# Optimization experiments

Hardware: AMD Instinct MI355X
Metric: run time of the kernel (lower is better)

## Reference

```python
import jax, jax.numpy as jnp
import numpy as np

N_HEADS = 16


def build_bd3lm_mask(n, block_size, dtype):
    """BD3LM mask for concatenated [xt | x0] input of length 2n.
    0 = attend, finfo.min = masked. Shape (2n, 2n)."""
    idx = jnp.arange(2 * n)
    q_idx = idx[:, None]
    kv_idx = idx[None, :]
    x0_q = q_idx >= n
    x0_kv = kv_idx >= n
    block_q = jnp.where(x0_q, (q_idx - n) // block_size, q_idx // block_size)
    block_kv = jnp.where(x0_kv, (kv_idx - n) // block_size, kv_idx // block_size)
    block_diagonal = (block_q == block_kv) & (x0_q == x0_kv)
    offset_block_causal = (block_q > block_kv) & x0_kv & (~x0_q)
    block_causal = (block_q >= block_kv) & x0_kv & x0_q
    can_attend = block_diagonal | offset_block_causal | block_causal
    neg = jnp.finfo(dtype).min
    return jnp.where(can_attend, jnp.array(0, dtype), jnp.array(neg, dtype))


def setup_inputs() -> dict:
    key = jax.random.key(0)
    ks = jax.random.split(key, 5)
    B, T, D = 4, 2048, 1024  # T = 2*L, L = 1024
    s = 1.0 / np.sqrt(D)
    return {
        "x": jax.random.normal(ks[0], (B, T, D), jnp.float32),
        "Wq": jax.random.normal(ks[1], (D, D), jnp.float32) * s,
        "bq": jnp.zeros((D,), jnp.float32),
        "Wk": jax.random.normal(ks[2], (D, D), jnp.float32) * s,
        "bk": jnp.zeros((D,), jnp.float32),
        "Wv": jax.random.normal(ks[3], (D, D), jnp.float32) * s,
        "bv": jnp.zeros((D,), jnp.float32),
        "Wo": jax.random.normal(ks[4], (D, D), jnp.float32) * s,
        "bo": jnp.zeros((D,), jnp.float32),
        "block_size": 4,
    }


def reference(x, Wq, bq, Wk, bk, Wv, bv, Wo, bo, block_size):
    B, T, D = x.shape
    H = N_HEADS
    hd = D // H
    n = T // 2  # length of each copy in [xt | x0]
    mask = build_bd3lm_mask(n, block_size, x.dtype)  # (T, T)

    def split_heads(t):  # (B, T, D) -> (B, H, T, hd)
        return t.reshape(B, T, H, hd).transpose(0, 2, 1, 3)

    q = split_heads(x @ Wq + bq) * (hd ** -0.5)
    k = split_heads(x @ Wk + bk)
    v = split_heads(x @ Wv + bv)
    scores = jnp.einsum("bhqd,bhkd->bhqk", q, k) + mask[None, None]
    attn = jax.nn.softmax(scores, axis=-1)
    ctx = jnp.einsum("bhqk,bhkd->bhqd", attn, v)
    ctx = ctx.transpose(0, 2, 1, 3).reshape(B, T, D)
    return ctx @ Wo + bo
```

## Files before the change

### kernel.cpp

```cpp
#include <hip/hip_runtime.h>
#include <hip/hip_bf16.h>
#include <stdint.h>

typedef __hip_bfloat16 bf16;
typedef short v8s __attribute__((ext_vector_type(8)));
typedef float v4f __attribute__((ext_vector_type(4)));

#define TT   2048
#define DD   1024
#define HH   16
#define HDIM 64
#define NN   1024
#define MASKV (-1e9f)
#define QSCALE 0.18033688011112042f

#if __has_builtin(__builtin_amdgcn_exp2f)
#define EXP2F(x) __builtin_amdgcn_exp2f(x)
#else
#define EXP2F(x) exp2f(x)
#endif

__device__ __forceinline__ v4f mfma16x16x32(v8s a, v8s b, v4f c) {
    return __builtin_amdgcn_mfma_f32_16x16x32_bf16(a, b, c, 0, 0, 0);
}

#define GLDS16(lds, g)                                                          \
    __builtin_amdgcn_global_load_lds(                                           \
        (const __attribute__((address_space(1))) void*)(g),                     \
        (__attribute__((address_space(3))) void*)(lds), 16, 0, 0)

__device__ __forceinline__ bf16 f2b(float f) { return __float2bfloat16(f); }

__global__ __launch_bounds__(256) void cast_x(const float* __restrict__ x,
                                              bf16* __restrict__ xb)
{
    const size_t i = ((size_t)blockIdx.x * 256 + threadIdx.x) * 4;
    const float4 f = *(const float4*)(x + i);
    union { bf16 b[4]; uint64_t u; } cv;
    cv.b[0] = f2b(f.x); cv.b[1] = f2b(f.y); cv.b[2] = f2b(f.z); cv.b[3] = f2b(f.w);
    *(uint64_t*)(xb + i) = cv.u;
}

__global__ __launch_bounds__(256) void transpose_w(
    const float* __restrict__ w0, const float* __restrict__ w1,
    const float* __restrict__ w2, const float* __restrict__ w3,
    bf16* __restrict__ dst)
{
    __shared__ float tile[64][65];
    const float* src = (blockIdx.z == 0) ? w0 : (blockIdx.z == 1) ? w1
                      : (blockIdx.z == 2) ? w2 : w3;
    bf16* d = dst + (size_t)blockIdx.z * 1024 * 1024;
    const int r0 = blockIdx.y * 64, c0 = blockIdx.x * 64;
    const int tx = threadIdx.x, ty = threadIdx.y;
#pragma unroll
    for (int j = 0; j < 16; j++) {
        int r = ty + j * 4;
        tile[r][tx] = src[(size_t)(r0 + r) * 1024 + c0 + tx];
    }
    __syncthreads();
#pragma unroll
    for (int j = 0; j < 16; j++) {
        int r = ty + j * 4;
        d[(size_t)(c0 + r) * 1024 + r0 + tx] = f2b(tile[tx][r]);
    }
}

__global__ __launch_bounds__(256) void transpose_v(
    const bf16* __restrict__ vtmp, bf16* __restrict__ vt)
{
    __shared__ bf16 tile[64][66];
    const int bh = blockIdx.y, t0 = blockIdx.x * 64;
    const int tx = threadIdx.x, ty = threadIdx.y;
    const bf16* src = vtmp + (size_t)bh * TT * HDIM;
    bf16* dst = vt + (size_t)bh * HDIM * TT;
#pragma unroll
    for (int j = 0; j < 16; j++) {
        int r = ty + j * 4;
        tile[r][tx] = src[(size_t)(t0 + r) * HDIM + tx];
    }
    __syncthreads();
#pragma unroll
    for (int j = 0; j < 16; j++) {
        int r = ty + j * 4;
        dst[(size_t)r * TT + t0 + tx] = tile[tx][r];
    }
}

__device__ __forceinline__ void gemm_core_256x128(
    const bf16* __restrict__ A, const bf16* __restrict__ BT,
    const int m0, const int n0, const int K,
    bf16* __restrict__ As, bf16* __restrict__ Bs,
    v4f (&acc)[8][2])
{
    const int tid  = threadIdx.x;
    const int lane = tid & 63, wv = tid >> 6;
    const int quad = lane >> 4, c = lane & 15;
    const int wm = wv >> 2, wn = wv & 3;
    const int c7 = c & 7;
    const int NT = K >> 6;

    const int rloc = wv * 8 + (lane >> 3);
    const int gsw  = ((lane & 7) ^ ((lane >> 3) & 7)) << 3;
    const bf16* aSrc = A  + (size_t)(m0 + rloc) * K + gsw;
    const bf16* bSrc = BT + (size_t)(n0 + rloc) * K + gsw;

#pragma unroll
    for (int i = 0; i < 8; i++)
#pragma unroll
        for (int j = 0; j < 2; j++) acc[i][j] = (v4f){0.f, 0.f, 0.f, 0.f};

    auto stageA = [&](bf16* dst, int j, int kt) {
        const int mo = ((j & 1) << 7) | ((j >> 1) << 6);
        GLDS16(dst + (j * 64 + wv * 8) * 64, aSrc + (size_t)mo * K + kt * 64);
    };
    auto stageB = [&](bf16* dst, int j, int kt) {
        GLDS16(dst + (j * 64 + wv * 8) * 64, bSrc + (size_t)(j << 6) * K + kt * 64);
    };

    stageB(Bs, 0, 0); stageB(Bs, 1, 0);
    stageA(As, 0, 0); stageA(As, 1, 0); stageA(As, 2, 0); stageA(As, 3, 0);
    asm volatile("s_waitcnt vmcnt(2)" ::: "memory");
    asm volatile("s_barrier" ::: "memory");

#pragma unroll 1
    for (int kt = 0; kt < NT; ++kt) {
        bf16* Ac = As + (kt & 1) * 16384;
        bf16* Bc = Bs + (kt & 1) * 8192;
        bf16* An = As + ((kt & 1) ^ 1) * 16384;
        bf16* Bn = Bs + ((kt & 1) ^ 1) * 8192;
        const int ktn = (kt + 1 < NT) ? kt + 1 : kt;

        v8s bfr[2][2];
#pragma unroll
        for (int nt = 0; nt < 2; nt++)
#pragma unroll
            for (int kh = 0; kh < 2; kh++)
                bfr[nt][kh] = *(const v8s*)(Bc + (wn * 32 + nt * 16 + c) * 64
                                            + (((kh * 4 + quad) ^ c7) << 3));
        v8s af[4][2];
#pragma unroll
        for (int mt = 0; mt < 4; mt++)
#pragma unroll
            for (int kh = 0; kh < 2; kh++)
                af[mt][kh] = *(const v8s*)(Ac + (wm * 64 + mt * 16 + c) * 64
                                           + (((kh * 4 + quad) ^ c7) << 3));
        stageB(Bn, 0, ktn); stageB(Bn, 1, ktn); stageA(An, 0, ktn);
        asm volatile("s_barrier" ::: "memory");
        __builtin_amdgcn_s_setprio(1);
#pragma unroll
        for (int mt = 0; mt < 4; mt++)
#pragma unroll
            for (int nt = 0; nt < 2; nt++) {
                acc[mt][nt] = mfma16x16x32(af[mt][0], bfr[nt][0], acc[mt][nt]);
                acc[mt][nt] = mfma16x16x32(af[mt][1], bfr[nt][1], acc[mt][nt]);
            }
        __builtin_amdgcn_s_setprio(0);
        asm volatile("s_waitcnt vmcnt(3)" ::: "memory");
        asm volatile("s_barrier" ::: "memory");

#pragma unroll
        for (int mt = 0; mt < 4; mt++)
#pragma unroll
            for (int kh = 0; kh < 2; kh++)
                af[mt][kh] = *(const v8s*)(Ac + (128 + wm * 64 + mt * 16 + c) * 64
                                           + (((kh * 4 + quad) ^ c7) << 3));
        stageA(An, 1, ktn); stageA(An, 2, ktn); stageA(An, 3, ktn);
        asm volatile("s_barrier" ::: "memory");
        __builtin_amdgcn_s_setprio(1);
#pragma unroll
        for (int mt = 0; mt < 4; mt++)
#pragma unroll
            for (int nt = 0; nt < 2; nt++) {
                acc[4 + mt][nt] = mfma16x16x32(af[mt][0], bfr[nt][0], acc[4 + mt][nt]);
                acc[4 + mt][nt] = mfma16x16x32(af[mt][1], bfr[nt][1], acc[4 + mt][nt]);
            }
        __builtin_amdgcn_s_setprio(0);
        asm volatile("s_waitcnt vmcnt(2)" ::: "memory");
        asm volatile("s_barrier" ::: "memory");
    }
}

__global__ __launch_bounds__(512, 2) void gemm_qkv(
    const bf16* __restrict__ A, const bf16* __restrict__ BT,
    const float* __restrict__ bq, const float* __restrict__ bk,
    const float* __restrict__ bv,
    bf16* __restrict__ qo, bf16* __restrict__ ko, bf16* __restrict__ vo)
{
    __shared__ __align__(16) bf16 As[2 * 256 * 64];
    __shared__ __align__(16) bf16 Bs[2 * 128 * 64];
    const int id  = blockIdx.x;
    const int fid = (id & 7) * 96 + (id >> 3);
    const int by  = fid / 24, bx = fid - by * 24;
    const int m0  = by * 256, n0 = bx * 128;

    v4f acc[8][2];
    gemm_core_256x128(A, BT, m0, n0, 1024, As, Bs, acc);

    const int tid  = threadIdx.x;
    const int lane = tid & 63, wv = tid >> 6;
    const int quad = lane >> 4, c = lane & 15;
    const int wm = wv >> 2, wn = wv & 3;

    const int type = n0 >> 10;
    bf16* o = (type == 0) ? qo : (type == 1) ? ko : vo;
    const float* bp = (type == 0) ? bq : (type == 1) ? bk : bv;
    const float scale = (type == 0) ? QSCALE : 1.0f;
    const int nbase = n0 & 1023;

#pragma unroll
    for (int mt = 0; mt < 8; mt++)
#pragma unroll
        for (int nt = 0; nt < 2; nt++) {
            const int within = nbase + wn * 32 + nt * 16 + c;
            const int h = within >> 6, d = within & 63;
            const float bias = bp[within];
#pragma unroll
            for (int r = 0; r < 4; r++) {
                const int row = m0 + wm * 128 + mt * 16 + quad * 4 + r;
                const int b_ = row >> 11, t = row & 2047;
                const int bh = b_ * HH + h;
                o[((size_t)bh * TT + t) * HDIM + d] =
                    f2b((acc[mt][nt][r] + bias) * scale);
            }
        }
}

__global__ __launch_bounds__(512, 2) void gemm_out(
    const bf16* __restrict__ A, const bf16* __restrict__ BT,
    const float* __restrict__ bo, float* __restrict__ out)
{
    __shared__ __align__(16) bf16 As[2 * 256 * 64];
    __shared__ __align__(16) bf16 Bs[2 * 128 * 64];
    const int id  = blockIdx.x;
    const int fid = (id & 7) * 32 + (id >> 3);
    const int by  = fid >> 3, bx = fid & 7;
    const int m0  = by * 256, n0 = bx * 128;

    v4f acc[8][2];
    gemm_core_256x128(A, BT, m0, n0, 1024, As, Bs, acc);

    const int tid  = threadIdx.x;
    const int lane = tid & 63, wv = tid >> 6;
    const int quad = lane >> 4, c = lane & 15;
    const int wm = wv >> 2, wn = wv & 3;

#pragma unroll
    for (int mt = 0; mt < 8; mt++)
#pragma unroll
        for (int nt = 0; nt < 2; nt++) {
            const int col = n0 + wn * 32 + nt * 16 + c;
            const float bias = bo[col];
#pragma unroll
            for (int r = 0; r < 4; r++) {
                const int row = m0 + wm * 128 + mt * 16 + quad * 4 + r;
                out[(size_t)row * 1024 + col] = acc[mt][nt][r] + bias;
            }
        }
}

__global__ __launch_bounds__(256, 4) void attn(
    const bf16* __restrict__ Q, const bf16* __restrict__ Kb,
    const bf16* __restrict__ VT, bf16* __restrict__ ctx,
    const int* __restrict__ bsp)
{
    __shared__ __align__(16) bf16 Kt[2][32 * 64];
    __shared__ __align__(16) bf16 Vt[2][64 * 32];
    __shared__ __align__(16) bf16 plds[4][2][16 * 32];

    const int bs = bsp[0];
    const float inv  = 1.0f / (float)bs;
    const float hinv = 0.5f * inv;
    const int tid = threadIdx.x, lane = tid & 63, wv = tid >> 6;
    const int quad = lane >> 4, c = lane & 15;
    const int bh = blockIdx.x & 63;
    const int j  = blockIdx.x >> 6;
    const int g_tbl[16] = {7,6,5,4, 0,1,2,3, 4,5,6,7, 3,2,1,0};
    const bool xt = j < 8;
    const int g  = g_tbl[j];
    const int q0g = (xt ? 0 : NN) + g * 128;

    const bf16* qp = Q  + (size_t)bh * TT * HDIM;
    const bf16* kp = Kb + (size_t)bh * TT * HDIM;
    const bf16* vp = VT + (size_t)bh * HDIM * TT;

    int d_lo = 0, nd = 0, nf = 0, b_lo = 0, nb = 0;
    if (xt) {
        d_lo = (bs * (q0g / bs)) & ~31;
        const int d_hi = min((bs * ((q0g + 127) / bs) + bs + 31) & ~31, NN);
        nd = (d_hi - d_lo) >> 5;
        const int f = bs * (q0g / bs);
        nf = f >> 5;
        b_lo = NN + (nf << 5);
        const int b_hi = NN + min((bs * ((q0g + 127) / bs) + 31) & ~31, NN);
        nb = (b_hi > b_lo) ? (b_hi - b_lo) >> 5 : 0;
    } else {
        const int q0l = q0g - NN;
        const int f = min(bs * (q0l / bs) + bs, NN);
        nf = f >> 5;
        b_lo = NN + (nf << 5);
        const int b_hi = NN + min((bs * ((q0l + 127) / bs) + bs + 31) & ~31, NN);
        nb = (b_hi > b_lo) ? (b_hi - b_lo) >> 5 : 0;
    }
    const int nc = nd + nf + nb;

    float bqv[2][4];
#pragma unroll
    for (int t = 0; t < 2; t++)
#pragma unroll
        for (int r = 0; r < 4; r++) {
            const int qrow = q0g + wv * 32 + t * 16 + quad * 4 + r;
            const int qloc = xt ? qrow : qrow - NN;
            bqv[t][r] = floorf(fmaf((float)qloc, inv, hinv));
        }

    v8s aq[2][2];
#pragma unroll
    for (int t = 0; t < 2; t++) {
        const int rowb = q0g + wv * 32 + t * 16;
        aq[t][0] = *(const v8s*)(qp + (size_t)(rowb + c) * HDIM + quad * 8);
        aq[t][1] = *(const v8s*)(qp + (size_t)(rowb + c) * HDIM + 32 + quad * 8);
    }

    v4f O[2][4];
#pragma unroll
    for (int t = 0; t < 2; t++)
#pragma unroll
        for (int dt = 0; dt < 4; dt++) O[t][dt] = (v4f){0.f, 0.f, 0.f, 0.f};
    float lr[2][4] = {{0.f,0.f,0.f,0.f},{0.f,0.f,0.f,0.f}};

    const int klrow = lane >> 3, ks8 = lane & 7;
    const bf16* kSrc0 = kp + (size_t)(wv * 8 + klrow) * HDIM + ((ks8 ^ klrow) << 3);
    const int vlrow = lane >> 2, vs8 = lane & 3;
    const bf16* vSrc0 = vp + (size_t)(wv * 16 + vlrow) * TT + ((vs8 ^ (vlrow & 3)) << 3);

    auto kb_of = [&](int i, int& kb, int& type) {
        if (i < nd)           { kb = d_lo + (i << 5);             type = 1; }
        else if (i < nd + nf) { kb = NN + ((i - nd) << 5);        type = 0; }
        else                  { kb = b_lo + ((i - nd - nf) << 5); type = xt ? 2 : 3; }
    };
    auto stage = [&](int i) {
        int kb, ty; kb_of(i, kb, ty);
        const int sel = i & 1;
        GLDS16(&Kt[sel][wv * 512], kSrc0 + (size_t)kb * HDIM);
        GLDS16(&Vt[sel][wv * 512], vSrc0 + kb);
    };

    stage(0);
    asm volatile("s_waitcnt vmcnt(0)" ::: "memory");
    asm volatile("s_barrier" ::: "memory");

    const int xk = c & 7, xv = c & 3;
    const int pquad = quad << 3;
#pragma unroll 1
    for (int i = 0; i < nc; i++) {
        int kb, type; kb_of(i, kb, type);
        const int sel = i & 1;
        const bf16* Kl = Kt[sel];
        const bf16* Vl = Vt[sel];

        const v8s k0a = *(const v8s*)(Kl + c * 64        + ((quad       ^ xk) << 3));
        const v8s k0b = *(const v8s*)(Kl + c * 64        + (((quad ^ 4) ^ xk) << 3));
        const v8s k1a = *(const v8s*)(Kl + (16 + c) * 64 + ((quad       ^ xk) << 3));
        const v8s k1b = *(const v8s*)(Kl + (16 + c) * 64 + (((quad ^ 4) ^ xk) << 3));
        v8s vf[4];
#pragma unroll
        for (int dt = 0; dt < 4; dt++)
            vf[dt] = *(const v8s*)(Vl + (dt * 16 + c) * 32 + ((quad ^ xv) << 3));

        if (i + 1 < nc) stage(i + 1);

        float bkA = 0.f, bkB = 0.f;
        if (type) {
            const int off = (type == 1) ? 0 : NN;
            bkA = floorf(fmaf((float)(kb + c - off),      inv, hinv));
            bkB = floorf(fmaf((float)(kb + 16 + c - off), inv, hinv));
        }

#pragma unroll
        for (int t = 0; t < 2; t++) {
            v4f Sa = (v4f){0.f, 0.f, 0.f, 0.f};
            v4f Sb = (v4f){0.f, 0.f, 0.f, 0.f};
            Sa = mfma16x16x32(aq[t][0], k0a, Sa);
            Sa = mfma16x16x32(aq[t][1], k0b, Sa);
            Sb = mfma16x16x32(aq[t][0], k1a, Sb);
            Sb = mfma16x16x32(aq[t][1], k1b, Sb);
            bf16* pw = &plds[wv][t][(quad * 4) * 32];
#pragma unroll
            for (int r = 0; r < 4; r++) {
                float sa = Sa[r], sb = Sb[r];
                if (type == 1) {
                    if (bkA != bqv[t][r]) sa = MASKV;
                    if (bkB != bqv[t][r]) sb = MASKV;
                } else if (type == 2) {
                    if (!(bkA < bqv[t][r])) sa = MASKV;
                    if (!(bkB < bqv[t][r])) sb = MASKV;
                } else if (type == 3) {
                    if (!(bkA <= bqv[t][r])) sa = MASKV;
                    if (!(bkB <= bqv[t][r])) sb = MASKV;
                }
                const float pa = EXP2F(sa);
                const float pb = EXP2F(sb);
                lr[t][r] += pa + pb;
                pw[r * 32 + (c ^ pquad)]        = f2b(pa);
                pw[r * 32 + ((c + 16) ^ pquad)] = f2b(pb);
            }
        }
        asm volatile("s_waitcnt lgkmcnt(0)" ::: "memory");
#pragma unroll
        for (int t = 0; t < 2; t++) {
            const v8s pf = *(const v8s*)(&plds[wv][t][c * 32 +
                                        ((quad ^ ((c >> 2) & 3)) << 3)]);
#pragma unroll
            for (int dt = 0; dt < 4; dt++)
                O[t][dt] = mfma16x16x32(pf, vf[dt], O[t][dt]);
        }

        asm volatile("s_waitcnt vmcnt(0)" ::: "memory");
        asm volatile("s_barrier" ::: "memory");
    }

    const int b_ = bh >> 4, h = bh & 15;
#pragma unroll
    for (int t = 0; t < 2; t++)
#pragma unroll
        for (int r = 0; r < 4; r++) {
            float s = lr[t][r];
#pragma unroll
            for (int off = 1; off < 16; off <<= 1) s += __shfl_xor(s, off);
            const float invl = 1.0f / fmaxf(s, 1e-30f);
            const int trow = q0g + wv * 32 + t * 16 + quad * 4 + r;
#pragma unroll
            for (int dt = 0; dt < 4; dt++)
                ctx[((size_t)(b_ * TT + trow)) * DD + h * 64 + dt * 16 + c] =
                    f2b(O[t][dt][r] * invl);
        }
}

extern "C" void kernel_launch(void* const* d_in, const int* in_sizes, int n_in,
                              void* d_out, int out_size, void* d_ws, size_t ws_size,
                              hipStream_t stream)
{
    const float* x  = (const float*)d_in[0];
    const float* Wq = (const float*)d_in[1];
    const float* bq = (const float*)d_in[2];
    const float* Wk = (const float*)d_in[3];
    const float* bk = (const float*)d_in[4];
    const float* Wv = (const float*)d_in[5];
    const float* bv = (const float*)d_in[6];
    const float* Wo = (const float*)d_in[7];
    const float* bo = (const float*)d_in[8];
    const int*  bsp = (const int*)d_in[9];
    float* out = (float*)d_out;

    bf16* ws    = (bf16*)d_ws;
    bf16* xb    = ws;
    bf16* wqkvT = xb + 8388608;
    bf16* woT   = wqkvT + 3 * 1024 * 1024;
    bf16* qbuf  = woT + 1024 * 1024;
    bf16* kbuf  = qbuf + 8388608;
    bf16* vtmp  = kbuf + 8388608;
    bf16* vt    = vtmp + 8388608;
    bf16* ctx   = xb;

    cast_x<<<8192, 256, 0, stream>>>(x, xb);
    transpose_w<<<dim3(16, 16, 4), dim3(64, 4), 0, stream>>>(Wq, Wk, Wv, Wo, wqkvT);
    gemm_qkv<<<768, 512, 0, stream>>>(xb, wqkvT, bq, bk, bv, qbuf, kbuf, vtmp);
    transpose_v<<<dim3(32, 64), dim3(64, 4), 0, stream>>>(vtmp, vt);
    attn<<<1024, 256, 0, stream>>>(qbuf, kbuf, vt, ctx, bsp);
    gemm_out<<<256, 512, 0, stream>>>(ctx, woT, bo, out);
}
```

Measured before the change: 244.6 us.

## Retile QKV GEMM to 256x192 blocks with a custom four-phase pipeline

After: 239.4 us. 2.1% less time.

```diff
diff --git a/kernel.cpp b/kernel.cpp
--- a/kernel.cpp
+++ b/kernel.cpp
@@ -86,6 +86,167 @@
     }
 }
 
+__global__ __launch_bounds__(512, 2) void gemm_qkv(
+    const bf16* __restrict__ A, const bf16* __restrict__ BT,
+    const float* __restrict__ bq, const float* __restrict__ bk,
+    const float* __restrict__ bv,
+    bf16* __restrict__ qo, bf16* __restrict__ ko, bf16* __restrict__ vo)
+{
+    __shared__ __align__(16) bf16 As[2 * 256 * 64];
+    __shared__ __align__(16) bf16 Bs[2 * 192 * 64];
+    const int K = 1024, NT = K >> 6;
+
+    const int id  = blockIdx.x;
+    const int fid = (id & 7) * 64 + (id >> 3);
+    const int by  = fid >> 4, bx = fid & 15;
+    const int m0  = by * 256, n0 = bx * 192;
+
+    const int tid  = threadIdx.x;
+    const int lane = tid & 63, wv = tid >> 6;
+    const int quad = lane >> 4, c = lane & 15;
+    const int wm = wv >> 2, wn = wv & 3;
+    const int c7 = c & 15 & 7;
+
+    const int q8  = lane >> 3;
+    const int gsw = ((lane & 7) ^ (q8 & 7)) << 3;
+    const bf16* aSrc = A + (size_t)(m0 + wv * 8 + q8) * K + gsw;
+    const int vB = wv * 8 + q8;
+    const bf16* bSrc = BT + (size_t)(n0 + (vB >> 4) * 48 + (vB & 15)) * K + gsw;
+
+    auto stageA = [&](bf16* dst, int j, int kt) {
+        GLDS16(dst + (j * 64 + wv * 8) * 64, aSrc + (size_t)(j * 64) * K + kt * 64);
+    };
+    auto stageB = [&](bf16* dst, int j, int kt) {
+        GLDS16(dst + (j * 64 + wv * 8) * 64, bSrc + (size_t)(j * 16) * K + kt * 64);
+    };
+
+    v4f acc[8][3];
+#pragma unroll
+    for (int i = 0; i < 8; i++)
+#pragma unroll
+        for (int j = 0; j < 3; j++) acc[i][j] = (v4f){0.f, 0.f, 0.f, 0.f};
+
+    stageB(Bs, 0, 0); stageB(Bs, 1, 0);
+    stageA(As, 0, 0); stageA(As, 2, 0);
+    stageA(As, 1, 0); stageA(As, 3, 0);
+    stageB(Bs, 2, 0);
+    asm volatile("s_waitcnt vmcnt(3)" ::: "memory");
+    asm volatile("s_barrier" ::: "memory");
+
+    v8s afr[4][2], bfr01[2][2], bfr2[2];
+#pragma unroll 1
+    for (int kt = 0; kt < NT; ++kt) {
+        bf16* Ac = As + (kt & 1) * 16384;
+        bf16* Bc = Bs + (kt & 1) * 12288;
+        bf16* An = As + ((kt & 1) ^ 1) * 16384;
+        bf16* Bn = Bs + ((kt & 1) ^ 1) * 12288;
+        const int ktn = (kt + 1 < NT) ? kt + 1 : kt;
+
+#pragma unroll
+        for (int nt = 0; nt < 2; nt++)
+#pragma unroll
+            for (int kh = 0; kh < 2; kh++)
+                bfr01[nt][kh] = *(const v8s*)(Bc + (nt * 64 + wn * 16 + c) * 64
+                                              + (((kh * 4 + quad) ^ c7) << 3));
+#pragma unroll
+        for (int mt = 0; mt < 4; mt++)
+#pragma unroll
+            for (int kh = 0; kh < 2; kh++)
+                afr[mt][kh] = *(const v8s*)(Ac + (wm * 128 + mt * 16 + c) * 64
+                                            + (((kh * 4 + quad) ^ c7) << 3));
+        stageB(Bn, 0, ktn); stageB(Bn, 1, ktn);
+        asm volatile("s_barrier" ::: "memory");
+        __builtin_amdgcn_s_setprio(1);
+#pragma unroll
+        for (int mt = 0; mt < 4; mt++)
+#pragma unroll
+            for (int nt = 0; nt < 2; nt++) {
+                acc[mt][nt] = mfma16x16x32(afr[mt][0], bfr01[nt][0], acc[mt][nt]);
+                acc[mt][nt] = mfma16x16x32(afr[mt][1], bfr01[nt][1], acc[mt][nt]);
+            }
+        __builtin_amdgcn_s_setprio(0);
+        asm volatile("s_waitcnt vmcnt(3)" ::: "memory");
+        asm volatile("s_barrier" ::: "memory");
+
+#pragma unroll
+        for (int mt = 0; mt < 4; mt++)
+#pragma unroll
+            for (int kh = 0; kh < 2; kh++)
+                afr[mt][kh] = *(const v8s*)(Ac + (wm * 128 + 64 + mt * 16 + c) * 64
+                                            + (((kh * 4 + quad) ^ c7) << 3));
+        stageA(An, 0, ktn); stageA(An, 2, ktn);
+        asm volatile("s_barrier" ::: "memory");
+        __builtin_amdgcn_s_setprio(1);
+#pragma unroll
+        for (int mt = 0; mt < 4; mt++)
+#pragma unroll
+            for (int nt = 0; nt < 2; nt++) {
+                acc[4 + mt][nt] = mfma16x16x32(afr[mt][0], bfr01[nt][0], acc[4 + mt][nt]);
+                acc[4 + mt][nt] = mfma16x16x32(afr[mt][1], bfr01[nt][1], acc[4 + mt][nt]);
+            }
+        __builtin_amdgcn_s_setprio(0);
+        asm volatile("s_waitcnt vmcnt(4)" ::: "memory");
+        asm volatile("s_barrier" ::: "memory");
+
+#pragma unroll
+        for (int kh = 0; kh < 2; kh++)
+            bfr2[kh] = *(const v8s*)(Bc + (128 + wn * 16 + c) * 64
+                                     + (((kh * 4 + quad) ^ c7) << 3));
+        stageA(An, 1, ktn); stageA(An, 3, ktn);
+        asm volatile("s_barrier" ::: "memory");
+        __builtin_amdgcn_s_setprio(1);
+#pragma unroll
+        for (int mt = 0; mt < 4; mt++) {
+            acc[4 + mt][2] = mfma16x16x32(afr[mt][0], bfr2[0], acc[4 + mt][2]);
+            acc[4 + mt][2] = mfma16x16x32(afr[mt][1], bfr2[1], acc[4 + mt][2]);
+        }
+        __builtin_amdgcn_s_setprio(0);
+        asm volatile("s_barrier" ::: "memory");
+
+#pragma unroll
+        for (int mt = 0; mt < 4; mt++)
+#pragma unroll
+            for (int kh = 0; kh < 2; kh++)
+                afr[mt][kh] = *(const v8s*)(Ac + (wm * 128 + mt * 16 + c) * 64
+                                            + (((kh * 4 + quad) ^ c7) << 3));
+        stageB(Bn, 2, ktn);
+        asm volatile("s_barrier" ::: "memory");
+        __builtin_amdgcn_s_setprio(1);
+#pragma unroll
+        for (int mt = 0; mt < 4; mt++) {
+            acc[mt][2] = mfma16x16x32(afr[mt][0], bfr2[0], acc[mt][2]);
+            acc[mt][2] = mfma16x16x32(afr[mt][1], bfr2[1], acc[mt][2]);
+        }
+        __builtin_amdgcn_s_setprio(0);
+        asm volatile("s_waitcnt vmcnt(3)" ::: "memory");
+        asm volatile("s_barrier" ::: "memory");
+    }
+    asm volatile("s_waitcnt vmcnt(0)" ::: "memory");
+
+#pragma unroll
+    for (int i = 0; i < 8; i++)
+#pragma unroll
+        for (int nt = 0; nt < 3; nt++) {
+            const int colb = n0 + wn * 48 + nt * 16;
+            const int type = colb >> 10;
+            bf16* o = (type == 0) ? qo : (type == 1) ? ko : vo;
+            const float* bp = (type == 0) ? bq : (type == 1) ? bk : bv;
+            const float scale = (type == 0) ? QSCALE : 1.0f;
+            const int within = (colb & 1023) + c;
+            const int h = within >> 6, d = within & 63;
+            const float bias = bp[within];
+#pragma unroll
+            for (int r = 0; r < 4; r++) {
+                const int row = m0 + wm * 128 + (i >> 2) * 64 + (i & 3) * 16
+                                + quad * 4 + r;
+                const int b_ = row >> 11, t = row & 2047;
+                const int bh = b_ * HH + h;
+                o[((size_t)bh * TT + t) * HDIM + d] =
+                    f2b((acc[i][nt][r] + bias) * scale);
+            }
+        }
+}
+
 __device__ __forceinline__ void gemm_core_256x128(
     const bf16* __restrict__ A, const bf16* __restrict__ BT,
     const int m0, const int n0, const int K,
@@ -178,51 +339,6 @@
         asm volatile("s_waitcnt vmcnt(2)" ::: "memory");
         asm volatile("s_barrier" ::: "memory");
     }
-}
-
-__global__ __launch_bounds__(512, 2) void gemm_qkv(
-    const bf16* __restrict__ A, const bf16* __restrict__ BT,
-    const float* __restrict__ bq, const float* __restrict__ bk,
-    const float* __restrict__ bv,
-    bf16* __restrict__ qo, bf16* __restrict__ ko, bf16* __restrict__ vo)
-{
-    __shared__ __align__(16) bf16 As[2 * 256 * 64];
-    __shared__ __align__(16) bf16 Bs[2 * 128 * 64];
-    const int id  = blockIdx.x;
-    const int fid = (id & 7) * 96 + (id >> 3);
-    const int by  = fid / 24, bx = fid - by * 24;
-    const int m0  = by * 256, n0 = bx * 128;
-
-    v4f acc[8][2];
-    gemm_core_256x128(A, BT, m0, n0, 1024, As, Bs, acc);
-
-    const int tid  = threadIdx.x;
-    const int lane = tid & 63, wv = tid >> 6;
-    const int quad = lane >> 4, c = lane & 15;
-    const int wm = wv >> 2, wn = wv & 3;
-
-    const int type = n0 >> 10;
-    bf16* o = (type == 0) ? qo : (type == 1) ? ko : vo;
-    const float* bp = (type == 0) ? bq : (type == 1) ? bk : bv;
-    const float scale = (type == 0) ? QSCALE : 1.0f;
-    const int nbase = n0 & 1023;
-
-#pragma unroll
-    for (int mt = 0; mt < 8; mt++)
-#pragma unroll
-        for (int nt = 0; nt < 2; nt++) {
-            const int within = nbase + wn * 32 + nt * 16 + c;
-            const int h = within >> 6, d = within & 63;
-            const float bias = bp[within];
-#pragma unroll
-            for (int r = 0; r < 4; r++) {
-                const int row = m0 + wm * 128 + mt * 16 + quad * 4 + r;
-                const int b_ = row >> 11, t = row & 2047;
-                const int bh = b_ * HH + h;
-                o[((size_t)bh * TT + t) * HDIM + d] =
-                    f2b((acc[mt][nt][r] + bias) * scale);
-            }
-        }
 }
 
 __global__ __launch_bounds__(512, 2) void gemm_out(
@@ -464,7 +580,7 @@
 
     cast_x<<<8192, 256, 0, stream>>>(x, xb);
     transpose_w<<<dim3(16, 16, 4), dim3(64, 4), 0, stream>>>(Wq, Wk, Wv, Wo, wqkvT);
-    gemm_qkv<<<768, 512, 0, stream>>>(xb, wqkvT, bq, bk, bv, qbuf, kbuf, vtmp);
+    gemm_qkv<<<512, 512, 0, stream>>>(xb, wqkvT, bq, bk, bv, qbuf, kbuf, vtmp);
     transpose_v<<<dim3(32, 64), dim3(64, 4), 0, stream>>>(vtmp, vt);
     attn<<<1024, 256, 0, stream>>>(qbuf, kbuf, vt, ctx, bsp);
     gemm_out<<<256, 512, 0, stream>>>(ctx, woT, bo, out);
```

## Retile GEMM core into templated 256xN tiles with finer-grained staged pipeline

Applied to the files above, without the earlier changes.

Result: slower. 270.6 us (+10.6%).

```diff
diff --git a/kernel.cpp b/kernel.cpp
--- a/kernel.cpp
+++ b/kernel.cpp
@@ -86,98 +86,119 @@
     }
 }
 
-__device__ __forceinline__ void gemm_core_256x128(
+template<int NB>
+__device__ __forceinline__ void gemm_core_mt(
     const bf16* __restrict__ A, const bf16* __restrict__ BT,
-    const int m0, const int n0, const int K,
+    const int m0, const int n0,
     bf16* __restrict__ As, bf16* __restrict__ Bs,
-    v4f (&acc)[8][2])
-{
+    v4f (&acc)[4][2 * NB])
+{
+    constexpr int K = 1024, NT = K >> 6, NTS = 2 * NB;
+    constexpr int BHALF = NB * 64 * 64;
     const int tid  = threadIdx.x;
     const int lane = tid & 63, wv = tid >> 6;
     const int quad = lane >> 4, c = lane & 15;
-    const int wm = wv >> 2, wn = wv & 3;
+    const int wm = wv >> 1, wn = wv & 1;
     const int c7 = c & 7;
-    const int NT = K >> 6;
-
-    const int rloc = wv * 8 + (lane >> 3);
-    const int gsw  = ((lane & 7) ^ ((lane >> 3) & 7)) << 3;
-    const bf16* aSrc = A  + (size_t)(m0 + rloc) * K + gsw;
-    const bf16* bSrc = BT + (size_t)(n0 + rloc) * K + gsw;
-
-#pragma unroll
-    for (int i = 0; i < 8; i++)
-#pragma unroll
-        for (int j = 0; j < 2; j++) acc[i][j] = (v4f){0.f, 0.f, 0.f, 0.f};
+
+    const int q8 = lane >> 3, rr = wv * 8 + q8;
+    const int gsw = ((lane & 7) ^ q8) << 3;
+    const bf16* aSrc = A  + (size_t)(m0 + (rr >> 4) * 64 + (rr & 15)) * K + gsw;
+    const bf16* bSrc = BT + (size_t)(n0 + rr) * K + gsw;
 
     auto stageA = [&](bf16* dst, int j, int kt) {
-        const int mo = ((j & 1) << 7) | ((j >> 1) << 6);
-        GLDS16(dst + (j * 64 + wv * 8) * 64, aSrc + (size_t)mo * K + kt * 64);
+        GLDS16(dst + (j * 64 + wv * 8) * 64, aSrc + (size_t)(j * 16) * K + kt * 64);
     };
     auto stageB = [&](bf16* dst, int j, int kt) {
-        GLDS16(dst + (j * 64 + wv * 8) * 64, bSrc + (size_t)(j << 6) * K + kt * 64);
+        GLDS16(dst + (j * 64 + wv * 8) * 64, bSrc + (size_t)(j * 64) * K + kt * 64);
     };
 
-    stageB(Bs, 0, 0); stageB(Bs, 1, 0);
-    stageA(As, 0, 0); stageA(As, 1, 0); stageA(As, 2, 0); stageA(As, 3, 0);
-    asm volatile("s_waitcnt vmcnt(2)" ::: "memory");
+#pragma unroll
+    for (int i = 0; i < 4; i++)
+#pragma unroll
+        for (int j = 0; j < NTS; j++) acc[i][j] = (v4f){0.f, 0.f, 0.f, 0.f};
+
+#pragma unroll
+    for (int j = 0; j < NB; j++) stageB(Bs, j, 0);
+#pragma unroll
+    for (int j = 0; j < 4; j++)  stageA(As, j, 0);
+    asm volatile("s_waitcnt vmcnt(3)" ::: "memory");
     asm volatile("s_barrier" ::: "memory");
 
 #pragma unroll 1
     for (int kt = 0; kt < NT; ++kt) {
         bf16* Ac = As + (kt & 1) * 16384;
-        bf16* Bc = Bs + (kt & 1) * 8192;
+        bf16* Bc = Bs + (kt & 1) * BHALF;
         bf16* An = As + ((kt & 1) ^ 1) * 16384;
-        bf16* Bn = Bs + ((kt & 1) ^ 1) * 8192;
+        bf16* Bn = Bs + ((kt & 1) ^ 1) * BHALF;
         const int ktn = (kt + 1 < NT) ? kt + 1 : kt;
 
-        v8s bfr[2][2];
-#pragma unroll
-        for (int nt = 0; nt < 2; nt++)
+        stageB(Bn, 0, ktn); stageB(Bn, 1, ktn);
+        v8s bfr[NTS][2];
+#pragma unroll
+        for (int nt = 0; nt < NTS; nt++)
 #pragma unroll
             for (int kh = 0; kh < 2; kh++)
-                bfr[nt][kh] = *(const v8s*)(Bc + (wn * 32 + nt * 16 + c) * 64
+                bfr[nt][kh] = *(const v8s*)(Bc + (wn * (NB * 32) + nt * 16 + c) * 64
                                             + (((kh * 4 + quad) ^ c7) << 3));
-        v8s af[4][2];
-#pragma unroll
-        for (int mt = 0; mt < 4; mt++)
-#pragma unroll
-            for (int kh = 0; kh < 2; kh++)
-                af[mt][kh] = *(const v8s*)(Ac + (wm * 64 + mt * 16 + c) * 64
-                                           + (((kh * 4 + quad) ^ c7) << 3));
-        stageB(Bn, 0, ktn); stageB(Bn, 1, ktn); stageA(An, 0, ktn);
+        v8s af0, af1;
+        af0 = *(const v8s*)(Ac + (0 * 64 + wm * 16 + c) * 64 + (((0 + quad) ^ c7) << 3));
+        af1 = *(const v8s*)(Ac + (0 * 64 + wm * 16 + c) * 64 + (((4 + quad) ^ c7) << 3));
+        __builtin_amdgcn_s_setprio(1);
+#pragma unroll
+        for (int nt = 0; nt < NTS; nt++) {
+            acc[0][nt] = mfma16x16x32(af0, bfr[nt][0], acc[0][nt]);
+            acc[0][nt] = mfma16x16x32(af1, bfr[nt][1], acc[0][nt]);
+        }
+        __builtin_amdgcn_s_setprio(0);
+        asm volatile("s_waitcnt vmcnt(4)" ::: "memory");
         asm volatile("s_barrier" ::: "memory");
+
+        if constexpr (NB == 3) { stageB(Bn, 2, ktn); stageA(An, 0, ktn); }
+        else                   { stageA(An, 0, ktn); stageA(An, 1, ktn); }
+        af0 = *(const v8s*)(Ac + (1 * 64 + wm * 16 + c) * 64 + (((0 + quad) ^ c7) << 3));
+        af1 = *(const v8s*)(Ac + (1 * 64 + wm * 16 + c) * 64 + (((4 + quad) ^ c7) << 3));
         __builtin_amdgcn_s_setprio(1);
 #pragma unroll
-        for (int mt = 0; mt < 4; mt++)
-#pragma unroll
-            for (int nt = 0; nt < 2; nt++) {
-                acc[mt][nt] = mfma16x16x32(af[mt][0], bfr[nt][0], acc[mt][nt]);
-                acc[mt][nt] = mfma16x16x32(af[mt][1], bfr[nt][1], acc[mt][nt]);
-            }
+        for (int nt = 0; nt < NTS; nt++) {
+            acc[1][nt] = mfma16x16x32(af0, bfr[nt][0], acc[1][nt]);
+            acc[1][nt] = mfma16x16x32(af1, bfr[nt][1], acc[1][nt]);
+        }
+        __builtin_amdgcn_s_setprio(0);
+        asm volatile("s_waitcnt vmcnt(5)" ::: "memory");
+        asm volatile("s_barrier" ::: "memory");
+
+        if constexpr (NB == 3) { stageA(An, 1, ktn); stageA(An, 2, ktn); }
+        else                   { stageA(An, 2, ktn); }
+        af0 = *(const v8s*)(Ac + (2 * 64 + wm * 16 + c) * 64 + (((0 + quad) ^ c7) << 3));
+        af1 = *(const v8s*)(Ac + (2 * 64 + wm * 16 + c) * 64 + (((4 + quad) ^ c7) << 3));
+        __builtin_amdgcn_s_setprio(1);
+#pragma unroll
+        for (int nt = 0; nt < NTS; nt++) {
+            acc[2][nt] = mfma16x16x32(af0, bfr[nt][0], acc[2][nt]);
+            acc[2][nt] = mfma16x16x32(af1, bfr[nt][1], acc[2][nt]);
+        }
+        __builtin_amdgcn_s_setprio(0);
+        if constexpr (NB == 3)
+            asm volatile("s_waitcnt vmcnt(6)" ::: "memory");
+        else
+            asm volatile("s_waitcnt vmcnt(5)" ::: "memory");
+        asm volatile("s_barrier" ::: "memory");
+
+        stageA(An, 3, ktn);
+        af0 = *(const v8s*)(Ac + (3 * 64 + wm * 16 + c) * 64 + (((0 + quad) ^ c7) << 3));
+        af1 = *(const v8s*)(Ac + (3 * 64 + wm * 16 + c) * 64 + (((4 + quad) ^ c7) << 3));
+        __builtin_amdgcn_s_setprio(1);
+#pragma unroll
+        for (int nt = 0; nt < NTS; nt++) {
+            acc[3][nt] = mfma16x16x32(af0, bfr[nt][0], acc[3][nt]);
+            acc[3][nt] = mfma16x16x32(af1, bfr[nt][1], acc[3][nt]);
+        }
         __builtin_amdgcn_s_setprio(0);
         asm volatile("s_waitcnt vmcnt(3)" ::: "memory");
         asm volatile("s_barrier" ::: "memory");
-
-#pragma unroll
-        for (int mt = 0; mt < 4; mt++)
-#pragma unroll
-            for (int kh = 0; kh < 2; kh++)
-                af[mt][kh] = *(const v8s*)(Ac + (128 + wm * 64 + mt * 16 + c) * 64
-                                           + (((kh * 4 + quad) ^ c7) << 3));
-        stageA(An, 1, ktn); stageA(An, 2, ktn); stageA(An, 3, ktn);
-        asm volatile("s_barrier" ::: "memory");
-        __builtin_amdgcn_s_setprio(1);
-#pragma unroll
-        for (int mt = 0; mt < 4; mt++)
-#pragma unroll
-            for (int nt = 0; nt < 2; nt++) {
-                acc[4 + mt][nt] = mfma16x16x32(af[mt][0], bfr[nt][0], acc[4 + mt][nt]);
-                acc[4 + mt][nt] = mfma16x16x32(af[mt][1], bfr[nt][1], acc[4 + mt][nt]);
-            }
-        __builtin_amdgcn_s_setprio(0);
-        asm volatile("s_waitcnt vmcnt(2)" ::: "memory");
-        asm volatile("s_barrier" ::: "memory");
-    }
+    }
+    asm volatile("s_waitcnt vmcnt(0)" ::: "memory");
 }
 
 __global__ __launch_bounds__(512, 2) void gemm_qkv(
@@ -187,40 +208,39 @@
     bf16* __restrict__ qo, bf16* __restrict__ ko, bf16* __restrict__ vo)
 {
     __shared__ __align__(16) bf16 As[2 * 256 * 64];
-    __shared__ __align__(16) bf16 Bs[2 * 128 * 64];
+    __shared__ __align__(16) bf16 Bs[2 * 192 * 64];
     const int id  = blockIdx.x;
-    const int fid = (id & 7) * 96 + (id >> 3);
-    const int by  = fid / 24, bx = fid - by * 24;
-    const int m0  = by * 256, n0 = bx * 128;
-
-    v4f acc[8][2];
-    gemm_core_256x128(A, BT, m0, n0, 1024, As, Bs, acc);
+    const int fid = (id & 7) * 64 + (id >> 3);
+    const int by  = fid >> 4, bx = fid & 15;
+    const int m0  = by * 256, n0 = bx * 192;
+
+    v4f acc[4][6];
+    gemm_core_mt<3>(A, BT, m0, n0, As, Bs, acc);
 
     const int tid  = threadIdx.x;
     const int lane = tid & 63, wv = tid >> 6;
     const int quad = lane >> 4, c = lane & 15;
-    const int wm = wv >> 2, wn = wv & 3;
-
-    const int type = n0 >> 10;
-    bf16* o = (type == 0) ? qo : (type == 1) ? ko : vo;
-    const float* bp = (type == 0) ? bq : (type == 1) ? bk : bv;
-    const float scale = (type == 0) ? QSCALE : 1.0f;
-    const int nbase = n0 & 1023;
-
-#pragma unroll
-    for (int mt = 0; mt < 8; mt++)
-#pragma unroll
-        for (int nt = 0; nt < 2; nt++) {
-            const int within = nbase + wn * 32 + nt * 16 + c;
+    const int wm = wv >> 1, wn = wv & 1;
+
+#pragma unroll
+    for (int p = 0; p < 4; p++)
+#pragma unroll
+        for (int nt = 0; nt < 6; nt++) {
+            const int colb = n0 + wn * 96 + nt * 16;
+            const int type = colb >> 10;
+            bf16* o = (type == 0) ? qo : (type == 1) ? ko : vo;
+            const float* bp = (type == 0) ? bq : (type == 1) ? bk : bv;
+            const float scale = (type == 0) ? QSCALE : 1.0f;
+            const int within = (colb & 1023) + c;
             const int h = within >> 6, d = within & 63;
             const float bias = bp[within];
 #pragma unroll
             for (int r = 0; r < 4; r++) {
-                const int row = m0 + wm * 128 + mt * 16 + quad * 4 + r;
+                const int row = m0 + wm * 64 + p * 16 + quad * 4 + r;
                 const int b_ = row >> 11, t = row & 2047;
                 const int bh = b_ * HH + h;
                 o[((size_t)bh * TT + t) * HDIM + d] =
-                    f2b((acc[mt][nt][r] + bias) * scale);
+                    f2b((acc[p][nt][r] + bias) * scale);
             }
         }
 }
@@ -236,24 +256,24 @@
     const int by  = fid >> 3, bx = fid & 7;
     const int m0  = by * 256, n0 = bx * 128;
 
-    v4f acc[8][2];
-    gemm_core_256x128(A, BT, m0, n0, 1024, As, Bs, acc);
+    v4f acc[4][4];
+    gemm_core_mt<2>(A, BT, m0, n0, As, Bs, acc);
 
     const int tid  = threadIdx.x;
     const int lane = tid & 63, wv = tid >> 6;
     const int quad = lane >> 4, c = lane & 15;
-    const int wm = wv >> 2, wn = wv & 3;
-
-#pragma unroll
-    for (int mt = 0; mt < 8; mt++)
-#pragma unroll
-        for (int nt = 0; nt < 2; nt++) {
-            const int col = n0 + wn * 32 + nt * 16 + c;
+    const int wm = wv >> 1, wn = wv & 1;
+
+#pragma unroll
+    for (int p = 0; p < 4; p++)
+#pragma unroll
+        for (int nt = 0; nt < 4; nt++) {
+            const int col = n0 + wn * 64 + nt * 16 + c;
             const float bias = bo[col];
 #pragma unroll
             for (int r = 0; r < 4; r++) {
-                const int row = m0 + wm * 128 + mt * 16 + quad * 4 + r;
-                out[(size_t)row * 1024 + col] = acc[mt][nt][r] + bias;
+                const int row = m0 + wm * 64 + p * 16 + quad * 4 + r;
+                out[(size_t)row * 1024 + col] = acc[p][nt][r] + bias;
             }
         }
 }
@@ -464,7 +484,7 @@
 
     cast_x<<<8192, 256, 0, stream>>>(x, xb);
     transpose_w<<<dim3(16, 16, 4), dim3(64, 4), 0, stream>>>(Wq, Wk, Wv, Wo, wqkvT);
-    gemm_qkv<<<768, 512, 0, stream>>>(xb, wqkvT, bq, bk, bv, qbuf, kbuf, vtmp);
+    gemm_qkv<<<512, 512, 0, stream>>>(xb, wqkvT, bq, bk, bv, qbuf, kbuf, vtmp);
     transpose_v<<<dim3(32, 64), dim3(64, 4), 0, stream>>>(vtmp, vt);
     attn<<<1024, 256, 0, stream>>>(qbuf, kbuf, vt, ctx, bsp);
     gemm_out<<<256, 512, 0, stream>>>(ctx, woT, bo, out);
```

## Fuse V transpose into QKV GEMM epilogue via swapped MFMA operands

Applied to the files above, without the earlier changes.

Result: faster. 238.7 us (-2.4%).

```diff
diff --git a/kernel.cpp b/kernel.cpp
--- a/kernel.cpp
+++ b/kernel.cpp
@@ -24,6 +24,14 @@
     return __builtin_amdgcn_mfma_f32_16x16x32_bf16(a, b, c, 0, 0, 0);
 }
 
+template<bool SW>
+__device__ __forceinline__ v4f MM(v8s a, v8s b, v4f c) {
+    if constexpr (SW)
+        return __builtin_amdgcn_mfma_f32_16x16x32_bf16(b, a, c, 0, 0, 0);
+    else
+        return __builtin_amdgcn_mfma_f32_16x16x32_bf16(a, b, c, 0, 0, 0);
+}
+
 #define GLDS16(lds, g)                                                          \
     __builtin_amdgcn_global_load_lds(                                           \
         (const __attribute__((address_space(1))) void*)(g),                     \
@@ -65,27 +73,7 @@
     }
 }
 
-__global__ __launch_bounds__(256) void transpose_v(
-    const bf16* __restrict__ vtmp, bf16* __restrict__ vt)
-{
-    __shared__ bf16 tile[64][66];
-    const int bh = blockIdx.y, t0 = blockIdx.x * 64;
-    const int tx = threadIdx.x, ty = threadIdx.y;
-    const bf16* src = vtmp + (size_t)bh * TT * HDIM;
-    bf16* dst = vt + (size_t)bh * HDIM * TT;
-#pragma unroll
-    for (int j = 0; j < 16; j++) {
-        int r = ty + j * 4;
-        tile[r][tx] = src[(size_t)(t0 + r) * HDIM + tx];
-    }
-    __syncthreads();
-#pragma unroll
-    for (int j = 0; j < 16; j++) {
-        int r = ty + j * 4;
-        dst[(size_t)r * TT + t0 + tx] = tile[tx][r];
-    }
-}
-
+template<bool SW>
 __device__ __forceinline__ void gemm_core_256x128(
     const bf16* __restrict__ A, const bf16* __restrict__ BT,
     const int m0, const int n0, const int K,
@@ -151,8 +139,8 @@
         for (int mt = 0; mt < 4; mt++)
 #pragma unroll
             for (int nt = 0; nt < 2; nt++) {
-                acc[mt][nt] = mfma16x16x32(af[mt][0], bfr[nt][0], acc[mt][nt]);
-                acc[mt][nt] = mfma16x16x32(af[mt][1], bfr[nt][1], acc[mt][nt]);
+                acc[mt][nt] = MM<SW>(af[mt][0], bfr[nt][0], acc[mt][nt]);
+                acc[mt][nt] = MM<SW>(af[mt][1], bfr[nt][1], acc[mt][nt]);
             }
         __builtin_amdgcn_s_setprio(0);
         asm volatile("s_waitcnt vmcnt(3)" ::: "memory");
@@ -171,20 +159,21 @@
         for (int mt = 0; mt < 4; mt++)
 #pragma unroll
             for (int nt = 0; nt < 2; nt++) {
-                acc[4 + mt][nt] = mfma16x16x32(af[mt][0], bfr[nt][0], acc[4 + mt][nt]);
-                acc[4 + mt][nt] = mfma16x16x32(af[mt][1], bfr[nt][1], acc[4 + mt][nt]);
+                acc[4 + mt][nt] = MM<SW>(af[mt][0], bfr[nt][0], acc[4 + mt][nt]);
+                acc[4 + mt][nt] = MM<SW>(af[mt][1], bfr[nt][1], acc[4 + mt][nt]);
             }
         __builtin_amdgcn_s_setprio(0);
         asm volatile("s_waitcnt vmcnt(2)" ::: "memory");
         asm volatile("s_barrier" ::: "memory");
     }
+    asm volatile("s_waitcnt vmcnt(0)" ::: "memory");
 }
 
 __global__ __launch_bounds__(512, 2) void gemm_qkv(
     const bf16* __restrict__ A, const bf16* __restrict__ BT,
     const float* __restrict__ bq, const float* __restrict__ bk,
     const float* __restrict__ bv,
-    bf16* __restrict__ qo, bf16* __restrict__ ko, bf16* __restrict__ vo)
+    bf16* __restrict__ qo, bf16* __restrict__ ko, bf16* __restrict__ vt)
 {
     __shared__ __align__(16) bf16 As[2 * 256 * 64];
     __shared__ __align__(16) bf16 Bs[2 * 128 * 64];
@@ -192,37 +181,56 @@
     const int fid = (id & 7) * 96 + (id >> 3);
     const int by  = fid / 24, bx = fid - by * 24;
     const int m0  = by * 256, n0 = bx * 128;
+    const int type = n0 >> 10;
 
     v4f acc[8][2];
-    gemm_core_256x128(A, BT, m0, n0, 1024, As, Bs, acc);
+    if (type == 2) gemm_core_256x128<true >(A, BT, m0, n0, 1024, As, Bs, acc);
+    else           gemm_core_256x128<false>(A, BT, m0, n0, 1024, As, Bs, acc);
 
     const int tid  = threadIdx.x;
     const int lane = tid & 63, wv = tid >> 6;
     const int quad = lane >> 4, c = lane & 15;
     const int wm = wv >> 2, wn = wv & 3;
-
-    const int type = n0 >> 10;
-    bf16* o = (type == 0) ? qo : (type == 1) ? ko : vo;
-    const float* bp = (type == 0) ? bq : (type == 1) ? bk : bv;
-    const float scale = (type == 0) ? QSCALE : 1.0f;
     const int nbase = n0 & 1023;
 
-#pragma unroll
-    for (int mt = 0; mt < 8; mt++)
-#pragma unroll
-        for (int nt = 0; nt < 2; nt++) {
-            const int within = nbase + wn * 32 + nt * 16 + c;
-            const int h = within >> 6, d = within & 63;
-            const float bias = bp[within];
-#pragma unroll
-            for (int r = 0; r < 4; r++) {
-                const int row = m0 + wm * 128 + mt * 16 + quad * 4 + r;
-                const int b_ = row >> 11, t = row & 2047;
-                const int bh = b_ * HH + h;
-                o[((size_t)bh * TT + t) * HDIM + d] =
-                    f2b((acc[mt][nt][r] + bias) * scale);
+    if (type < 2) {
+        bf16* o = (type == 0) ? qo : ko;
+        const float* bp = (type == 0) ? bq : bk;
+        const float scale = (type == 0) ? QSCALE : 1.0f;
+#pragma unroll
+        for (int mt = 0; mt < 8; mt++)
+#pragma unroll
+            for (int nt = 0; nt < 2; nt++) {
+                const int within = nbase + wn * 32 + nt * 16 + c;
+                const int h = within >> 6, d = within & 63;
+                const float bias = bp[within];
+#pragma unroll
+                for (int r = 0; r < 4; r++) {
+                    const int row = m0 + wm * 128 + mt * 16 + quad * 4 + r;
+                    const int b_ = row >> 11, t = row & 2047;
+                    const int bh = b_ * HH + h;
+                    o[((size_t)bh * TT + t) * HDIM + d] =
+                        f2b((acc[mt][nt][r] + bias) * scale);
+                }
             }
-        }
+    } else {
+        const int b_    = m0 >> 11;
+        const int m0loc = m0 & 2047;
+#pragma unroll
+        for (int mt = 0; mt < 8; mt++) {
+            const int t = m0loc + wm * 128 + mt * 16 + c;
+#pragma unroll
+            for (int nt = 0; nt < 2; nt++)
+#pragma unroll
+                for (int r = 0; r < 4; r++) {
+                    const int within = nbase + wn * 32 + nt * 16 + quad * 4 + r;
+                    const int h = within >> 6, d = within & 63;
+                    const int bh = b_ * HH + h;
+                    vt[((size_t)bh * HDIM + d) * TT + t] =
+                        f2b(acc[mt][nt][r] + bv[within]);
+                }
+        }
+    }
 }
 
 __global__ __launch_bounds__(512, 2) void gemm_out(
@@ -237,7 +245,7 @@
     const int m0  = by * 256, n0 = bx * 128;
 
     v4f acc[8][2];
-    gemm_core_256x128(A, BT, m0, n0, 1024, As, Bs, acc);
+    gemm_core_256x128<false>(A, BT, m0, n0, 1024, As, Bs, acc);
 
     const int tid  = threadIdx.x;
     const int lane = tid & 63, wv = tid >> 6;
@@ -380,10 +388,12 @@
         for (int t = 0; t < 2; t++) {
             v4f Sa = (v4f){0.f, 0.f, 0.f, 0.f};
             v4f Sb = (v4f){0.f, 0.f, 0.f, 0.f};
+            __builtin_amdgcn_s_setprio(1);
             Sa = mfma16x16x32(aq[t][0], k0a, Sa);
             Sa = mfma16x16x32(aq[t][1], k0b, Sa);
             Sb = mfma16x16x32(aq[t][0], k1a, Sb);
             Sb = mfma16x16x32(aq[t][1], k1b, Sb);
+            __builtin_amdgcn_s_setprio(0);
             bf16* pw = &plds[wv][t][(quad * 4) * 32];
 #pragma unroll
             for (int r = 0; r < 4; r++) {
@@ -410,9 +420,11 @@
         for (int t = 0; t < 2; t++) {
             const v8s pf = *(const v8s*)(&plds[wv][t][c * 32 +
                                         ((quad ^ ((c >> 2) & 3)) << 3)]);
+            __builtin_amdgcn_s_setprio(1);
 #pragma unroll
             for (int dt = 0; dt < 4; dt++)
                 O[t][dt] = mfma16x16x32(pf, vf[dt], O[t][dt]);
+            __builtin_amdgcn_s_setprio(0);
         }
 
         asm volatile("s_waitcnt vmcnt(0)" ::: "memory");
@@ -458,14 +470,12 @@
     bf16* woT   = wqkvT + 3 * 1024 * 1024;
     bf16* qbuf  = woT + 1024 * 1024;
     bf16* kbuf  = qbuf + 8388608;
-    bf16* vtmp  = kbuf + 8388608;
-    bf16* vt    = vtmp + 8388608;
+    bf16* vt    = kbuf + 8388608;
     bf16* ctx   = xb;
 
     cast_x<<<8192, 256, 0, stream>>>(x, xb);
     transpose_w<<<dim3(16, 16, 4), dim3(64, 4), 0, stream>>>(Wq, Wk, Wv, Wo, wqkvT);
-    gemm_qkv<<<768, 512, 0, stream>>>(xb, wqkvT, bq, bk, bv, qbuf, kbuf, vtmp);
-    transpose_v<<<dim3(32, 64), dim3(64, 4), 0, stream>>>(vtmp, vt);
+    gemm_qkv<<<768, 512, 0, stream>>>(xb, wqkvT, bq, bk, bv, qbuf, kbuf, vt);
     attn<<<1024, 256, 0, stream>>>(qbuf, kbuf, vt, ctx, bsp);
     gemm_out<<<256, 512, 0, stream>>>(ctx, woT, bo, out);
 }
```
